# Kernel optimization log

Measured on AMD Instinct MI355X. Metric: run time of the kernel, lower is better.

The kernel has to match this reference:

```python
import jax, jax.numpy as jnp
import numpy as np

DIM = 1024
NUM_HEADS = 16
HEAD_DIM = DIM // NUM_HEADS
SCALE = HEAD_DIM ** -0.5


def setup_inputs() -> dict:
    key = jax.random.key(0)
    k1, k2, k3 = jax.random.split(key, 3)
    B, N = 2, 2048
    x = jax.random.normal(k1, (B, N, DIM), dtype=jnp.float32)
    # qkv: Linear(dim, 3*dim, bias=False); proj: Linear(dim, dim) with bias
    w_qkv = jax.random.normal(k2, (3 * DIM, DIM), dtype=jnp.float32) * (DIM ** -0.5)
    w_proj = jax.random.normal(k3, (DIM, DIM), dtype=jnp.float32) * (DIM ** -0.5)
    b_proj = jnp.zeros((DIM,), dtype=jnp.float32)
    return {"x": x, "w_qkv": w_qkv, "w_proj": w_proj, "b_proj": b_proj}


def reference(x, w_qkv, w_proj, b_proj):
    B, N, C = x.shape
    H, D = NUM_HEADS, HEAD_DIM
    qkv = jnp.einsum('bnc,fc->bnf', x, w_qkv)                 # [B,N,3C]
    qkv = qkv.reshape(B, N, 3, H, D).transpose(2, 0, 3, 1, 4)  # [3,B,H,N,D]
    q, k, v = qkv[0], qkv[1], qkv[2]
    q = q * SCALE
    attn = jnp.einsum('bhnd,bhmd->bhnm', q, k)                 # [B,H,N,N]
    attn = jax.nn.softmax(attn, axis=-1)
    out = jnp.einsum('bhnm,bhmd->bhnd', attn, v)               # [B,H,N,D]
    out = out.transpose(0, 2, 1, 3).reshape(B, N, C)
    out = jnp.einsum('bnc,fc->bnf', out, w_proj) + b_proj
    return out
```

## Files before the change

### kernel.cpp

```cpp
#include <hip/hip_runtime.h>
#include <hip/hip_bf16.h>
#include <stdint.h>

typedef __attribute__((ext_vector_type(4))) float f32x4;
typedef __attribute__((ext_vector_type(16))) float f32x16;
typedef __attribute__((ext_vector_type(8))) short bf16x8;
typedef __attribute__((ext_vector_type(4))) short bf16x4;
typedef unsigned short ushort_t;

#define QSCALE 0.18033688f

__device__ inline short f2bf(float f) {
  unsigned u = __builtin_bit_cast(unsigned, f);
  u += 0x7fffu + ((u >> 16) & 1u);
  return (short)(u >> 16);
}

__device__ inline void gload_lds16(const void* g, void* l) {
  __builtin_amdgcn_global_load_lds(
      (const __attribute__((address_space(1))) void*)g,
      (__attribute__((address_space(3))) void*)l, 16, 0, 0);
}

__device__ inline unsigned cvtpk(float a, float b) {
  unsigned r;
  asm("v_cvt_pk_bf16_f32 %0, %1, %2" : "=v"(r) : "v"(a), "v"(b));
  return r;
}

__device__ inline void swap32u(unsigned& a, unsigned& b) {
  asm("v_permlane32_swap_b32 %0, %1" : "+v"(a), "+v"(b));
}

__global__ __launch_bounds__(256) void cvt_all(const float* __restrict__ x,
                                               const float* __restrict__ wq,
                                               const float* __restrict__ wp,
                                               short* __restrict__ Xb,
                                               short* __restrict__ Wq,
                                               short* __restrict__ Wp) {
  int i = blockIdx.x * 256 + threadIdx.x;
  const float* s;
  short* d;
  int off;
  if (i < 524288)       { s = x;  d = Xb; off = i; }
  else if (i < 917504)  { s = wq; d = Wq; off = i - 524288; }
  else                  { s = wp; d = Wp; off = i - 917504; }
  const float4* sv = (const float4*)s;
  float4 a = sv[2 * off], b = sv[2 * off + 1];
  bf16x8 o;
  o[0] = f2bf(a.x); o[1] = f2bf(a.y); o[2] = f2bf(a.z); o[3] = f2bf(a.w);
  o[4] = f2bf(b.x); o[5] = f2bf(b.y); o[6] = f2bf(b.z); o[7] = f2bf(b.w);
  ((bf16x8*)d)[off] = o;
}

template <int F32OUT, int SPLITV>
__global__ __launch_bounds__(256, 2) void gemm_db(const short* __restrict__ A,
                                                  const short* __restrict__ B,
                                                  void* __restrict__ Cv,
                                                  short* __restrict__ Vtg,
                                                  const float* __restrict__ bias,
                                                  int scale_cols, float scale_val,
                                                  int M, int N, int K) {
  __shared__ short Ab[2][128 * 64];
  __shared__ short Bb[2][128 * 64];
  const int tid = threadIdx.x, wv = tid >> 6, ln = tid & 63;
  const int wm = wv >> 1, wn = wv & 1;
  const int bn0 = blockIdx.x * 128, bm0 = blockIdx.y * 128;
  const int nt = K >> 6;

  const int srow = ln >> 3;
  const int scol = ((ln & 7) ^ (ln >> 3)) * 8;
  const int fln = ln & 15;
  const int fk = ln >> 4;

  f32x4 acc[4][4] = {};

  auto stage = [&](int t, int s) {
    const size_t k0 = (size_t)t << 6;
#pragma unroll
    for (int rd = 0; rd < 4; rd++) {
      const int ch = 4 * wv + rd;
      gload_lds16(A + (size_t)(bm0 + ch * 8 + srow) * K + k0 + scol,
                  (char*)Ab[s] + ch * 1024);
      gload_lds16(B + (size_t)(bn0 + ch * 8 + srow) * K + k0 + scol,
                  (char*)Bb[s] + ch * 1024);
    }
  };

  stage(0, 0);
  stage(1, 1);
  asm volatile("s_waitcnt vmcnt(8)" ::: "memory");
  __builtin_amdgcn_s_barrier();
  __builtin_amdgcn_sched_barrier(0);

  for (int t = 0; t < nt; t++) {
    const int s = t & 1;
    const char* Ap = (const char*)Ab[s];
    const char* Bp = (const char*)Bb[s];

    bf16x8 af[4][2], bf[4][2];
#pragma unroll
    for (int m = 0; m < 4; m++) {
      const int R = wm * 64 + m * 16 + fln;
#pragma unroll
      for (int kk = 0; kk < 2; kk++)
        af[m][kk] = *(const bf16x8*)(Ap + R * 128 + ((((kk << 2) | fk) ^ (R & 7)) << 4));
    }
#pragma unroll
    for (int n = 0; n < 4; n++) {
      const int R = wn * 64 + n * 16 + fln;
#pragma unroll
      for (int kk = 0; kk < 2; kk++)
        bf[n][kk] = *(const bf16x8*)(Bp + R * 128 + ((((kk << 2) | fk) ^ (R & 7)) << 4));
    }

    __builtin_amdgcn_s_setprio(1);
#pragma unroll
    for (int kk = 0; kk < 2; kk++)
#pragma unroll
      for (int m = 0; m < 4; m++)
#pragma unroll
        for (int n = 0; n < 4; n++)
          acc[m][n] = __builtin_amdgcn_mfma_f32_16x16x32_bf16(af[m][kk], bf[n][kk], acc[m][n], 0, 0, 0);
    __builtin_amdgcn_s_setprio(0);

    if (t + 1 < nt) {
      __builtin_amdgcn_s_barrier();
      if (t + 2 < nt) {
        stage(t + 2, s);
        asm volatile("s_waitcnt vmcnt(8)" ::: "memory");
      } else {
        asm volatile("s_waitcnt vmcnt(0)" ::: "memory");
      }
      __builtin_amdgcn_s_barrier();
      __builtin_amdgcn_sched_barrier(0);
    }
  }

  const int r0 = bm0 + wm * 64, c0 = bn0 + wn * 64;
  const int fg4 = fk * 4;
#pragma unroll
  for (int m = 0; m < 4; m++) {
    const int row0 = r0 + m * 16 + fg4;
#pragma unroll
    for (int n = 0; n < 4; n++) {
      const int col = c0 + n * 16 + fln;
      if constexpr (SPLITV) {
        if (col < 2048) {
          const float sc = (col < scale_cols) ? scale_val : 1.0f;
#pragma unroll
          for (int j = 0; j < 4; j++)
            ((short*)Cv)[(size_t)(row0 + j) * 2048 + col] = f2bf(acc[m][n][j] * sc);
        } else {
          const int f = col - 2048, h = f >> 6, d = f & 63;
          const int bb = row0 >> 11, ntok = row0 & 2047;
          bf16x4 w;
#pragma unroll
          for (int j = 0; j < 4; j++) w[j] = f2bf(acc[m][n][j]);
          *(bf16x4*)(Vtg + ((size_t)((bb * 16 + h) * 64 + d)) * 2048 + ntok) = w;
        }
      } else {
#pragma unroll
        for (int j = 0; j < 4; j++) {
          float v = acc[m][n][j];
          if (col < scale_cols) v *= scale_val;
          if (F32OUT) ((float*)Cv)[(size_t)(row0 + j) * N + col] = v + bias[col];
          else        ((short*)Cv)[(size_t)(row0 + j) * N + col] = f2bf(v);
        }
      }
    }
  }
}

__global__ __launch_bounds__(256, 2) void attn_fwd(const short* __restrict__ QK,
                                                   const short* __restrict__ Vtg,
                                                   short* __restrict__ AO) {
  __shared__ short Ks[3][64 * 64];
  __shared__ short Vt[3][64 * 64];
  const int tid = threadIdx.x, wv = tid >> 6, ln = tid & 63;
  const int lq = ln & 31, hi = ln >> 5;
  const int id = blockIdx.x;
  const int c = (id & 7) * 64 + (id >> 3);
  const int qt = c & 15, bh = c >> 4;
  const int b = bh >> 4, h = bh & 15;
  const short* base = QK + (size_t)(b * 2048) * 2048 + h * 64;
  const short* Kg = base + 1024;
  const short* Vg = Vtg + (size_t)bh * 64 * 2048;
  const int qrow = qt * 128 + wv * 32 + lq;

  bf16x8 qf[4];
  {
    const short* Qrow = base + (size_t)qrow * 2048;
#pragma unroll
    for (int ds = 0; ds < 4; ds++)
      qf[ds] = *(const bf16x8*)(Qrow + ds * 16 + hi * 8);
  }

  const int krow = ln >> 3;
  const int kcol = ((ln & 7) ^ (ln >> 3)) * 8;

  float l_run = 0.f;
  f32x16 o0 = {}, o1 = {};

#define STAGE(t, s)                                                              \
  {                                                                              \
    _Pragma("unroll")                                                            \
    for (int rd = 0; rd < 2; rd++) {                                             \
      const int r8 = 16 * wv + 8 * rd + krow;                                    \
      gload_lds16(Kg + (size_t)((t) * 64 + r8) * 2048 + kcol,                    \
                  (char*)Ks[s] + (2 * wv + rd) * 1024);                          \
      gload_lds16(Vg + (size_t)r8 * 2048 + (t) * 64 + kcol,                      \
                  (char*)Vt[s] + (2 * wv + rd) * 1024);                          \
    }                                                                            \
  }

  STAGE(0, 0);
  STAGE(1, 1);

  for (int t = 0; t < 32; t++) {
    const int s = t % 3;
    if (t < 31) asm volatile("s_waitcnt vmcnt(4)" ::: "memory");
    else        asm volatile("s_waitcnt vmcnt(0)" ::: "memory");
    __builtin_amdgcn_s_barrier();
    __builtin_amdgcn_sched_barrier(0);
    if (t + 2 < 32) STAGE(t + 2, (t + 2) % 3);

    f32x16 c0 = {}, c1 = {};
    const char* Kb = (const char*)Ks[s];
    __builtin_amdgcn_s_setprio(1);
#pragma unroll
    for (int ds = 0; ds < 4; ds++) {
      const int cp = (ds * 2 + hi) ^ (lq & 7);
      bf16x8 ka0 = *(const bf16x8*)(Kb + lq * 128 + cp * 16);
      bf16x8 ka1 = *(const bf16x8*)(Kb + (32 + lq) * 128 + cp * 16);
      c0 = __builtin_amdgcn_mfma_f32_32x32x16_bf16(ka0, qf[ds], c0, 0, 0, 0);
      c1 = __builtin_amdgcn_mfma_f32_32x32x16_bf16(ka1, qf[ds], c1, 0, 0, 0);
    }
    __builtin_amdgcn_s_setprio(0);

#pragma unroll
    for (int r = 0; r < 16; r++) c0[r] = __builtin_amdgcn_exp2f(c0[r]);
#pragma unroll
    for (int r = 0; r < 16; r++) c1[r] = __builtin_amdgcn_exp2f(c1[r]);
    {
      float st[8];
#pragma unroll
      for (int r = 0; r < 8; r++)
        st[r] = (c0[2 * r] + c0[2 * r + 1]) + (c1[2 * r] + c1[2 * r + 1]);
#pragma unroll
      for (int r = 0; r < 4; r++) st[r] += st[r + 4];
      l_run += (st[0] + st[1]) + (st[2] + st[3]);
    }

    bf16x8 pa[4];
#pragma unroll
    for (int cs = 0; cs < 2; cs++) {
      const f32x16& p = cs ? c1 : c0;
#pragma unroll
      for (int ksl = 0; ksl < 2; ksl++) {
        unsigned A0 = cvtpk(p[8 * ksl + 0], p[8 * ksl + 1]);
        unsigned A1 = cvtpk(p[8 * ksl + 2], p[8 * ksl + 3]);
        unsigned B0 = cvtpk(p[8 * ksl + 4], p[8 * ksl + 5]);
        unsigned B1 = cvtpk(p[8 * ksl + 6], p[8 * ksl + 7]);
        swap32u(A0, B0);
        swap32u(A1, B1);
        union { unsigned u[4]; bf16x8 v; } tmp;
        tmp.u[0] = A0; tmp.u[1] = A1; tmp.u[2] = B0; tmp.u[3] = B1;
        pa[cs * 2 + ksl] = tmp.v;
      }
    }

    const char* Vb = (const char*)Vt[s];
    __builtin_amdgcn_s_setprio(1);
#pragma unroll
    for (int ks = 0; ks < 4; ks++) {
      const int cp = (ks * 2 + hi) ^ (lq & 7);
      bf16x8 va0 = *(const bf16x8*)(Vb + lq * 128 + cp * 16);
      bf16x8 va1 = *(const bf16x8*)(Vb + (32 + lq) * 128 + cp * 16);
      o0 = __builtin_amdgcn_mfma_f32_32x32x16_bf16(va0, pa[ks], o0, 0, 0, 0);
      o1 = __builtin_amdgcn_mfma_f32_32x32x16_bf16(va1, pa[ks], o1, 0, 0, 0);
    }
    __builtin_amdgcn_s_setprio(0);
  }
#undef STAGE

  l_run += __shfl_xor(l_run, 32);
  const float inv = __builtin_amdgcn_rcpf(l_run);
  short* Arow = AO + ((size_t)(b * 2048) + qrow) * 1024 + h * 64;
#pragma unroll
  for (int dt = 0; dt < 2; dt++) {
    const f32x16& o = dt ? o1 : o0;
#pragma unroll
    for (int g = 0; g < 4; g++) {
      bf16x4 w;
#pragma unroll
      for (int i = 0; i < 4; i++) w[i] = f2bf(o[4 * g + i] * inv);
      *(bf16x4*)(Arow + dt * 32 + 8 * g + 4 * hi) = w;
    }
  }
}

extern "C" void kernel_launch(void* const* d_in, const int* in_sizes, int n_in,
                              void* d_out, int out_size, void* d_ws, size_t ws_size,
                              hipStream_t stream) {
  const float* x = (const float*)d_in[0];
  const float* w_qkv = (const float*)d_in[1];
  const float* w_proj = (const float*)d_in[2];
  const float* b_proj = (const float*)d_in[3];
  float* out = (float*)d_out;

  char* ws = (char*)d_ws;
  short* Xb  = (short*)(ws + 0);
  short* Wq  = (short*)(ws + 8388608);
  short* Wp  = (short*)(ws + 14680064);
  short* QK  = (short*)(ws + 16777216);
  short* Vtg = (short*)(ws + 33554432);
  short* AO  = (short*)(ws + 41943040);

  cvt_all<<<4096, 256, 0, stream>>>(x, w_qkv, w_proj, Xb, Wq, Wp);

  gemm_db<0, 1><<<dim3(24, 32), 256, 0, stream>>>(Xb, Wq, QK, Vtg, nullptr,
                                                  1024, QSCALE, 4096, 3072, 1024);

  attn_fwd<<<dim3(512), 256, 0, stream>>>(QK, Vtg, AO);

  gemm_db<1, 0><<<dim3(8, 32), 256, 0, stream>>>(AO, Wp, out, nullptr, b_proj,
                                                 0, 1.0f, 4096, 1024, 1024);
}
```

Measured before the change: 115.6 us.

## Remap GEMM blocks per XCD and stage V transpose through LDS for coalesced stores

```diff
diff --git a/kernel.cpp b/kernel.cpp
--- a/kernel.cpp
+++ b/kernel.cpp
@@ -53,7 +53,7 @@
   ((bf16x8*)d)[off] = o;
 }
 
-template <int F32OUT, int SPLITV>
+template <int F32OUT, int SPLITV, int BXPX>
 __global__ __launch_bounds__(256, 2) void gemm_db(const short* __restrict__ A,
                                                   const short* __restrict__ B,
                                                   void* __restrict__ Cv,
@@ -61,11 +61,16 @@
                                                   const float* __restrict__ bias,
                                                   int scale_cols, float scale_val,
                                                   int M, int N, int K) {
-  __shared__ short Ab[2][128 * 64];
-  __shared__ short Bb[2][128 * 64];
+  __shared__ char smem[65536];
+  short* Ab0 = (short*)smem;
+  short* Bb0 = (short*)(smem + 32768);
   const int tid = threadIdx.x, wv = tid >> 6, ln = tid & 63;
   const int wm = wv >> 1, wn = wv & 1;
-  const int bn0 = blockIdx.x * 128, bm0 = blockIdx.y * 128;
+  const int id = blockIdx.x;
+  const int xcd = id & 7, local = id >> 3;
+  const int bx = xcd * BXPX + local % BXPX;
+  const int by = local / BXPX;
+  const int bn0 = bx * 128, bm0 = by * 128;
   const int nt = K >> 6;
 
   const int srow = ln >> 3;
@@ -81,9 +86,9 @@
     for (int rd = 0; rd < 4; rd++) {
       const int ch = 4 * wv + rd;
       gload_lds16(A + (size_t)(bm0 + ch * 8 + srow) * K + k0 + scol,
-                  (char*)Ab[s] + ch * 1024);
+                  (char*)(Ab0 + s * 8192) + ch * 1024);
       gload_lds16(B + (size_t)(bn0 + ch * 8 + srow) * K + k0 + scol,
-                  (char*)Bb[s] + ch * 1024);
+                  (char*)(Bb0 + s * 8192) + ch * 1024);
     }
   };
 
@@ -95,8 +100,8 @@
 
   for (int t = 0; t < nt; t++) {
     const int s = t & 1;
-    const char* Ap = (const char*)Ab[s];
-    const char* Bp = (const char*)Bb[s];
+    const char* Ap = (const char*)(Ab0 + s * 8192);
+    const char* Bp = (const char*)(Bb0 + s * 8192);
 
     bf16x8 af[4][2], bf[4][2];
 #pragma unroll
@@ -137,6 +142,36 @@
     }
   }
 
+  if constexpr (SPLITV) {
+    if (bn0 >= 2048) {
+      __syncthreads();
+      short* Vl = (short*)smem;
+#pragma unroll
+      for (int m = 0; m < 4; m++) {
+        const int tok0 = wm * 64 + m * 16 + fk * 4;
+#pragma unroll
+        for (int n = 0; n < 4; n++) {
+          const int f_loc = wn * 64 + n * 16 + fln;
+          bf16x4 w;
+#pragma unroll
+          for (int j = 0; j < 4; j++) w[j] = f2bf(acc[m][n][j]);
+          *(bf16x4*)(Vl + f_loc * 136 + tok0) = w;
+        }
+      }
+      __syncthreads();
+      const int fbase = bn0 - 2048, bb = bm0 >> 11, ntok0 = bm0 & 2047;
+#pragma unroll
+      for (int pass = 0; pass < 8; pass++) {
+        const int f_loc = wv * 32 + pass * 4 + (ln >> 4);
+        const int f = fbase + f_loc;
+        const int g = (bb * 16 + (f >> 6)) * 64 + (f & 63);
+        bf16x8 w = *(const bf16x8*)(Vl + f_loc * 136 + (ln & 15) * 8);
+        *(bf16x8*)(Vtg + (size_t)g * 2048 + ntok0 + (ln & 15) * 8) = w;
+      }
+      return;
+    }
+  }
+
   const int r0 = bm0 + wm * 64, c0 = bn0 + wn * 64;
   const int fg4 = fk * 4;
 #pragma unroll
@@ -146,19 +181,10 @@
     for (int n = 0; n < 4; n++) {
       const int col = c0 + n * 16 + fln;
       if constexpr (SPLITV) {
-        if (col < 2048) {
-          const float sc = (col < scale_cols) ? scale_val : 1.0f;
-#pragma unroll
-          for (int j = 0; j < 4; j++)
-            ((short*)Cv)[(size_t)(row0 + j) * 2048 + col] = f2bf(acc[m][n][j] * sc);
-        } else {
-          const int f = col - 2048, h = f >> 6, d = f & 63;
-          const int bb = row0 >> 11, ntok = row0 & 2047;
-          bf16x4 w;
-#pragma unroll
-          for (int j = 0; j < 4; j++) w[j] = f2bf(acc[m][n][j]);
-          *(bf16x4*)(Vtg + ((size_t)((bb * 16 + h) * 64 + d)) * 2048 + ntok) = w;
-        }
+        const float sc = (col < scale_cols) ? scale_val : 1.0f;
+#pragma unroll
+        for (int j = 0; j < 4; j++)
+          ((short*)Cv)[(size_t)(row0 + j) * 2048 + col] = f2bf(acc[m][n][j] * sc);
       } else {
 #pragma unroll
         for (int j = 0; j < 4; j++) {
@@ -319,11 +345,11 @@
 
   cvt_all<<<4096, 256, 0, stream>>>(x, w_qkv, w_proj, Xb, Wq, Wp);
 
-  gemm_db<0, 1><<<dim3(24, 32), 256, 0, stream>>>(Xb, Wq, QK, Vtg, nullptr,
+  gemm_db<0, 1, 3><<<dim3(768), 256, 0, stream>>>(Xb, Wq, QK, Vtg, nullptr,
                                                   1024, QSCALE, 4096, 3072, 1024);
 
   attn_fwd<<<dim3(512), 256, 0, stream>>>(QK, Vtg, AO);
 
-  gemm_db<1, 0><<<dim3(8, 32), 256, 0, stream>>>(AO, Wp, out, nullptr, b_proj,
-                                                 0, 1.0f, 4096, 1024, 1024);
-}
+  gemm_db<1, 0, 1><<<dim3(256), 256, 0, stream>>>(AO, Wp, out, nullptr, b_proj,
+                                                  0, 1.0f, 4096, 1024, 1024);
+}
```

New measurement: 103.1 us. -10.8%, faster.
